# Optimization experiments

Hardware: AMD Instinct MI355X
Metric: run time of the kernel (lower is better)

The kernel has to match this reference:

```python
import jax, jax.numpy as jnp
import numpy as np

B, N, M, D, H = 2, 1024, 1024, 768, 72  # H = num_layers*nhead = 6*12

def setup_inputs() -> dict:
    key = jax.random.key(0)
    ks = jax.random.split(key, 7)
    s = lambda fan_in: 1.0 / np.sqrt(fan_in)
    return {
        "x": jax.random.normal(ks[0], (B, N, D), dtype=jnp.float32),
        "stacked_scores": jax.random.normal(ks[1], (B, H, N, M), dtype=jnp.float32),
        "W1": jax.random.uniform(ks[2], (D, D // 2), jnp.float32, -s(D), s(D)),
        "b1": jax.random.uniform(ks[3], (D // 2,), jnp.float32, -s(D), s(D)),
        "W2": jax.random.uniform(ks[4], (D // 2, H), jnp.float32, -s(D // 2), s(D // 2)),
        "b2": jax.random.uniform(ks[5], (H,), jnp.float32, -s(D // 2), s(D // 2)),
        "bias": jnp.zeros((1,), dtype=jnp.float32),
    }

def reference(x, stacked_scores, W1, b1, W2, b2, bias):
    # Router MLP: Linear -> exact GELU -> Linear  => raw_weights [b, n, h]
    h = jax.nn.gelu(jnp.einsum('bnd,df->bnf', x, W1) + b1, approximate=False)
    raw_weights = jnp.einsum('bnf,fh->bnh', h, W2) + b2
    # Weighted combine of stacked attention maps, reducing over heads
    final_matrix = jnp.einsum('bnh,bhnm->bnm', raw_weights, stacked_scores)
    return final_matrix + bias
```

## Files before the change

### kernel.cpp

```cpp
#include <hip/hip_runtime.h>
#include <math.h>

#define B_ 2
#define N_ 1024
#define M_ 1024
#define D_ 768
#define F_ 384
#define H_ 72
#define ROWS 8
#define PFH 3

typedef float f32x4 __attribute__((ext_vector_type(4)));

__global__ __launch_bounds__(512) void fused_kernel(
    const float* __restrict__ x, const float* __restrict__ scores,
    const float* __restrict__ W1, const float* __restrict__ b1,
    const float* __restrict__ W2, const float* __restrict__ b2,
    const float* __restrict__ bias, float* __restrict__ out)
{
    const int t = threadIdx.x;
    const int blk = blockIdx.x;
    const int b = blk >> 7;
    const int n0 = (blk & 127) * ROWS;
    const int row0 = (b << 10) + n0;

    __shared__ float xs[ROWS][D_];
    __shared__ float hs[ROWS][F_ + 8];
    __shared__ float rwv[ROWS][80];
    __shared__ float pf[PFH][ROWS][M_];

    const f32x4* __restrict__ sp = reinterpret_cast<const f32x4*>(scores);
    const int hstr = N_ * (M_ / 4);
    const int sbase = ((b * H_) * N_ + n0) * (M_ / 4);

    if (t < 384) {
        const f32x4* xg = reinterpret_cast<const f32x4*>(x + row0 * D_);
        f32x4* xl = reinterpret_cast<f32x4*>(&xs[0][0]);
#pragma unroll
        for (int i = 0; i < 4; ++i)
            xl[t + i * 384] = xg[t + i * 384];
    }
    __syncthreads();

    if (t < 384) {
        const int f = t;
        float acc[ROWS];
#pragma unroll
        for (int r = 0; r < ROWS; ++r) acc[r] = 0.0f;

#pragma unroll 4
        for (int d = 0; d < D_; d += 4) {
            const float w0 = W1[(d + 0) * F_ + f];
            const float w1v = W1[(d + 1) * F_ + f];
            const float w2v = W1[(d + 2) * F_ + f];
            const float w3v = W1[(d + 3) * F_ + f];
#pragma unroll
            for (int r = 0; r < ROWS; ++r) {
                const float4 xv = *reinterpret_cast<const float4*>(&xs[r][d]);
                acc[r] = fmaf(xv.x, w0, acc[r]);
                acc[r] = fmaf(xv.y, w1v, acc[r]);
                acc[r] = fmaf(xv.z, w2v, acc[r]);
                acc[r] = fmaf(xv.w, w3v, acc[r]);
            }
        }
        const float bb = b1[f];
#pragma unroll
        for (int r = 0; r < ROWS; ++r) {
            const float v = acc[r] + bb;
            hs[r][f] = 0.5f * v * (1.0f + erff(v * 0.70710678118654752f));
        }
    } else {
        const int j = t - 384;
        f32x4* pfl = reinterpret_cast<f32x4*>(&pf[0][0][0]);
#pragma unroll 1
        for (int base_i = 0; base_i < PFH * ROWS * 256; base_i += 128 * 12) {
            f32x4 tmp[12];
#pragma unroll
            for (int u = 0; u < 12; ++u) {
                const int i = base_i + u * 128 + j;
                const int h = i >> 11;
                const int rem = i & 2047;
                tmp[u] = __builtin_nontemporal_load(sp + sbase + h * hstr + rem);
            }
#pragma unroll
            for (int u = 0; u < 12; ++u)
                pfl[base_i + u * 128 + j] = tmp[u];
        }
    }
    __syncthreads();

#pragma unroll 1
    for (int o = t; o < ROWS * H_; o += 512) {
        const int r = o / H_;
        const int c = o - r * H_;
        float s = 0.0f;
#pragma unroll 4
        for (int k = 0; k < F_; k += 4) {
            const float4 hv = *reinterpret_cast<const float4*>(&hs[r][k]);
            s = fmaf(hv.x, W2[(k + 0) * H_ + c], s);
            s = fmaf(hv.y, W2[(k + 1) * H_ + c], s);
            s = fmaf(hv.z, W2[(k + 2) * H_ + c], s);
            s = fmaf(hv.w, W2[(k + 3) * H_ + c], s);
        }
        rwv[r][c] = s + b2[c];
    }
    __syncthreads();

    const int col = t & 255;
    const int r0v = (t >> 8) * 4;

    const int base = sbase + r0v * (M_ / 4) + col;

    f32x4 a0 = 0.f, a1 = 0.f, a2 = 0.f, a3 = 0.f;
#pragma unroll 2
    for (int h = PFH; h < H_; ++h) {
        const int ib = base + h * hstr;
        const f32x4 v0 = __builtin_nontemporal_load(sp + ib);
        const f32x4 v1 = __builtin_nontemporal_load(sp + ib + 256);
        const f32x4 v2 = __builtin_nontemporal_load(sp + ib + 512);
        const f32x4 v3 = __builtin_nontemporal_load(sp + ib + 768);
        const float w0 = rwv[r0v + 0][h];
        const float w1 = rwv[r0v + 1][h];
        const float w2 = rwv[r0v + 2][h];
        const float w3 = rwv[r0v + 3][h];
#pragma unroll
        for (int j = 0; j < 4; ++j) {
            a0[j] = fmaf(w0, v0[j], a0[j]);
            a1[j] = fmaf(w1, v1[j], a1[j]);
            a2[j] = fmaf(w2, v2[j], a2[j]);
            a3[j] = fmaf(w3, v3[j], a3[j]);
        }
    }
#pragma unroll
    for (int h = 0; h < PFH; ++h) {
        const f32x4 v0 = *reinterpret_cast<const f32x4*>(&pf[h][r0v + 0][col * 4]);
        const f32x4 v1 = *reinterpret_cast<const f32x4*>(&pf[h][r0v + 1][col * 4]);
        const f32x4 v2 = *reinterpret_cast<const f32x4*>(&pf[h][r0v + 2][col * 4]);
        const f32x4 v3 = *reinterpret_cast<const f32x4*>(&pf[h][r0v + 3][col * 4]);
        const float w0 = rwv[r0v + 0][h];
        const float w1 = rwv[r0v + 1][h];
        const float w2 = rwv[r0v + 2][h];
        const float w3 = rwv[r0v + 3][h];
#pragma unroll
        for (int j = 0; j < 4; ++j) {
            a0[j] = fmaf(w0, v0[j], a0[j]);
            a1[j] = fmaf(w1, v1[j], a1[j]);
            a2[j] = fmaf(w2, v2[j], a2[j]);
            a3[j] = fmaf(w3, v3[j], a3[j]);
        }
    }

    const float bv = bias[0];
#pragma unroll
    for (int j = 0; j < 4; ++j) { a0[j] += bv; a1[j] += bv; a2[j] += bv; a3[j] += bv; }

    f32x4* __restrict__ op = reinterpret_cast<f32x4*>(out);
    const int obase = (row0 + r0v) * (M_ / 4) + col;
    __builtin_nontemporal_store(a0, op + obase);
    __builtin_nontemporal_store(a1, op + obase + 256);
    __builtin_nontemporal_store(a2, op + obase + 512);
    __builtin_nontemporal_store(a3, op + obase + 768);
}

extern "C" void kernel_launch(void* const* d_in, const int* in_sizes, int n_in,
                              void* d_out, int out_size, void* d_ws, size_t ws_size,
                              hipStream_t stream) {
    const float* x      = (const float*)d_in[0];
    const float* scores = (const float*)d_in[1];
    const float* W1     = (const float*)d_in[2];
    const float* b1     = (const float*)d_in[3];
    const float* W2     = (const float*)d_in[4];
    const float* b2     = (const float*)d_in[5];
    const float* bias   = (const float*)d_in[6];
    float* out = (float*)d_out;

    fused_kernel<<<(B_ * N_) / ROWS, 512, 0, stream>>>(
        x, scores, W1, b1, W2, b2, bias, out);
}
```

Baseline: 139.3 us.

## Rebalance warp roles: 128 threads compute MLP, 384 prefetch scores

Shrinks the GELU-MLP compute group from 384 threads (one output feature each) to 128 threads that each compute three features, reusing every shared-memory x read across three weight columns. The freed 384 threads prefetch the first score heads into shared memory, each issuing 16 outstanding loads in a single batch. All 512 threads now cooperate on loading x. The aim is more memory-level parallelism in the prefetch and fewer LDS reads per FMA in the MLP. The cost is much higher register pressure in both roles and a longer serial MLP stage on fewer threads.

```diff
diff --git a/kernel.cpp b/kernel.cpp
--- a/kernel.cpp
+++ b/kernel.cpp
@@ -33,59 +33,67 @@
     const int hstr = N_ * (M_ / 4);
     const int sbase = ((b * H_) * N_ + n0) * (M_ / 4);
 
-    if (t < 384) {
+    {
         const f32x4* xg = reinterpret_cast<const f32x4*>(x + row0 * D_);
         f32x4* xl = reinterpret_cast<f32x4*>(&xs[0][0]);
 #pragma unroll
-        for (int i = 0; i < 4; ++i)
-            xl[t + i * 384] = xg[t + i * 384];
+        for (int i = 0; i < 3; ++i)
+            xl[t + i * 512] = xg[t + i * 512];
     }
     __syncthreads();
 
-    if (t < 384) {
+    if (t < 128) {
         const int f = t;
-        float acc[ROWS];
+        float acc[3][ROWS];
 #pragma unroll
-        for (int r = 0; r < ROWS; ++r) acc[r] = 0.0f;
+        for (int c = 0; c < 3; ++c)
+#pragma unroll
+            for (int r = 0; r < ROWS; ++r) acc[c][r] = 0.0f;
 
-#pragma unroll 4
+#pragma unroll 2
         for (int d = 0; d < D_; d += 4) {
-            const float w0 = W1[(d + 0) * F_ + f];
-            const float w1v = W1[(d + 1) * F_ + f];
-            const float w2v = W1[(d + 2) * F_ + f];
-            const float w3v = W1[(d + 3) * F_ + f];
+            float wv[3][4];
+#pragma unroll
+            for (int c = 0; c < 3; ++c)
+#pragma unroll
+                for (int i = 0; i < 4; ++i)
+                    wv[c][i] = W1[(d + i) * F_ + f + c * 128];
 #pragma unroll
             for (int r = 0; r < ROWS; ++r) {
                 const float4 xv = *reinterpret_cast<const float4*>(&xs[r][d]);
-                acc[r] = fmaf(xv.x, w0, acc[r]);
-                acc[r] = fmaf(xv.y, w1v, acc[r]);
-                acc[r] = fmaf(xv.z, w2v, acc[r]);
-                acc[r] = fmaf(xv.w, w3v, acc[r]);
+#pragma unroll
+                for (int c = 0; c < 3; ++c) {
+                    acc[c][r] = fmaf(xv.x, wv[c][0], acc[c][r]);
+                    acc[c][r] = fmaf(xv.y, wv[c][1], acc[c][r]);
+                    acc[c][r] = fmaf(xv.z, wv[c][2], acc[c][r]);
+                    acc[c][r] = fmaf(xv.w, wv[c][3], acc[c][r]);
+                }
             }
         }
-        const float bb = b1[f];
 #pragma unroll
-        for (int r = 0; r < ROWS; ++r) {
-            const float v = acc[r] + bb;
-            hs[r][f] = 0.5f * v * (1.0f + erff(v * 0.70710678118654752f));
+        for (int c = 0; c < 3; ++c) {
+            const float bb = b1[f + c * 128];
+#pragma unroll
+            for (int r = 0; r < ROWS; ++r) {
+                const float v = acc[c][r] + bb;
+                hs[r][f + c * 128] =
+                    0.5f * v * (1.0f + erff(v * 0.70710678118654752f));
+            }
         }
     } else {
-        const int j = t - 384;
+        const int j = t - 128;
         f32x4* pfl = reinterpret_cast<f32x4*>(&pf[0][0][0]);
-#pragma unroll 1
-        for (int base_i = 0; base_i < PFH * ROWS * 256; base_i += 128 * 12) {
-            f32x4 tmp[12];
+        f32x4 tmp[16];
 #pragma unroll
-            for (int u = 0; u < 12; ++u) {
-                const int i = base_i + u * 128 + j;
-                const int h = i >> 11;
-                const int rem = i & 2047;
-                tmp[u] = __builtin_nontemporal_load(sp + sbase + h * hstr + rem);
-            }
+        for (int u = 0; u < 16; ++u) {
+            const int i = u * 384 + j;
+            const int h = i >> 11;
+            const int rem = i & 2047;
+            tmp[u] = __builtin_nontemporal_load(sp + sbase + h * hstr + rem);
+        }
 #pragma unroll
-            for (int u = 0; u < 12; ++u)
-                pfl[base_i + u * 128 + j] = tmp[u];
-        }
+        for (int u = 0; u < 16; ++u)
+            pfl[u * 384 + j] = tmp[u];
     }
     __syncthreads();
 
```

After: 144.6 us. 1.04x slower.
